# Kernel optimization log

Hardware: AMD Instinct MI355X
Metric: run time of the kernel (lower is better)

## Reference

```python
import jax, jax.numpy as jnp
import numpy as np

TEMPERATURE = 0.5
EPS = 1e-8  # matches torch CosineSimilarity eps


def setup_inputs() -> dict:
    key = jax.random.key(0)
    k1, k2 = jax.random.split(key)
    N, D = 4096, 256
    z1 = jax.random.normal(k1, (N, D), dtype=jnp.float32)
    z2 = jax.random.normal(k2, (N, D), dtype=jnp.float32)
    return {"z1": z1, "z2": z2}


def reference(z1, z2):
    N = z1.shape[0]
    z = jnp.concatenate([z1, z2], axis=0)            # [2N, D]
    norm = jnp.linalg.norm(z, axis=-1, keepdims=True)
    zn = z / jnp.maximum(norm, EPS)                  # L2-normalized
    sim = (zn @ zn.T) / TEMPERATURE                  # [2N, 2N] cosine sim / temp
    # mask self-similarity on the diagonal
    diag = jnp.eye(2 * N, dtype=bool)
    sim = jnp.where(diag, -jnp.inf, sim)
    # positive pair labels: row i pairs with i+N (first half) or i-N (second half)
    labels = jnp.concatenate([jnp.arange(N) + N, jnp.arange(N)])
    logp = jax.nn.log_softmax(sim, axis=-1)
    loss = -jnp.mean(logp[jnp.arange(2 * N), labels])
    return loss
```

## Files before the change

### kernel.cpp

```cpp
#include <hip/hip_runtime.h>
#include <hip/hip_bf16.h>


#define NROWS 8192
#define NHALF 4096
#define DDIM  256

typedef __bf16 bf16;
typedef __bf16 bf16x4 __attribute__((ext_vector_type(4)));
typedef __bf16 bf16x8 __attribute__((ext_vector_type(8)));
typedef float  f32x4  __attribute__((ext_vector_type(4)));

__constant__ const float kTwoLog2e = 2.8853900817779268f;
__constant__ const float kLn2      = 0.6931471805599453f;

__device__ __forceinline__ const float* zrow(const float* z1, const float* z2, int r) {
  return (r < NHALF) ? (z1 + (size_t)r * DDIM) : (z2 + (size_t)(r - NHALF) * DDIM);
}

__global__ void k_normalize(const float* __restrict__ z1, const float* __restrict__ z2,
                            bf16* __restrict__ zn, float* __restrict__ invn,
                            float* __restrict__ rowsum) {
  const int wave = threadIdx.x >> 6, lane = threadIdx.x & 63;
  const int row = blockIdx.x * 4 + wave;
  const float* src = zrow(z1, z2, row);
  f32x4 v = *(const f32x4*)(src + lane * 4);
  float ss = v.x * v.x + v.y * v.y + v.z * v.z + v.w * v.w;
#pragma unroll
  for (int off = 1; off < 64; off <<= 1) ss += __shfl_xor(ss, off);
  const float inv = 1.0f / fmaxf(sqrtf(ss), 1e-8f);
  bf16x4 o;
  o.x = (bf16)(v.x * inv); o.y = (bf16)(v.y * inv);
  o.z = (bf16)(v.z * inv); o.w = (bf16)(v.w * inv);
  *(bf16x4*)(zn + (size_t)row * DDIM + lane * 4) = o;
  if (lane == 0) { invn[row] = inv; rowsum[row] = 0.0f; }
}

#define BMG 256
#define BNG 32
#define CSPLIT 16

typedef const __attribute__((address_space(1))) unsigned int* as1_u32p;
typedef __attribute__((address_space(3))) unsigned int* as3_u32p;

__device__ __forceinline__ void load_lds16(const void* g, void* l) {
  __builtin_amdgcn_global_load_lds((as1_u32p)g, (as3_u32p)l, 16, 0, 0);
}

__global__ __launch_bounds__(256, 2) void k_gram(const bf16* __restrict__ zn,
                                                 float* __restrict__ rowsum) {
  __shared__ __align__(16) unsigned char ldsb[2][BNG * 512];
  const int tid  = threadIdx.x;
  const int wave = tid >> 6, lane = tid & 63;
  const int quad = lane >> 4, l15 = lane & 15;
  const int rowblk = blockIdx.x >> 4, csplit = blockIdx.x & 15;
  const int c0 = csplit * (NROWS / CSPLIT);
  const int iters = (NROWS / CSPLIT) / BNG;

  {
    const unsigned char* src0 = (const unsigned char*)(zn + (size_t)c0 * DDIM);
#pragma unroll
    for (int j = 0; j < 4; ++j) {
      const int p = (wave * 4 + j) * 64 + lane;
      const int r = p >> 5;
      const int q = (p & 31) ^ (r & 7);
      load_lds16(src0 + r * 512 + q * 16, &ldsb[0][(wave * 4 + j) * 1024]);
    }
  }

  const int R0 = rowblk * BMG + wave * 64;
  bf16x8 a[4][8];
#pragma unroll
  for (int s = 0; s < 4; ++s) {
    const bf16x8* ap = (const bf16x8*)(zn + (size_t)(R0 + s * 16 + l15) * DDIM);
#pragma unroll
    for (int kk = 0; kk < 8; ++kk) a[s][kk] = ap[kk * 4 + quad];
  }

  float sum[4][4];
#pragma unroll
  for (int s = 0; s < 4; ++s)
#pragma unroll
    for (int r = 0; r < 4; ++r) sum[s][r] = 0.0f;

  const f32x4 zero4 = {0.f, 0.f, 0.f, 0.f};

  for (int it = 0; it < iters; ++it) {
    __syncthreads();
    const unsigned char* bp = ldsb[it & 1];

    if (it + 1 < iters) {
      const unsigned char* srcn =
          (const unsigned char*)(zn + (size_t)(c0 + (it + 1) * BNG) * DDIM);
#pragma unroll
      for (int j = 0; j < 4; ++j) {
        const int p = (wave * 4 + j) * 64 + lane;
        const int r = p >> 5;
        const int q = (p & 31) ^ (r & 7);
        load_lds16(srcn + r * 512 + q * 16, &ldsb[(it + 1) & 1][(wave * 4 + j) * 1024]);
      }
    }

    f32x4 acc[4][2];
#pragma unroll
    for (int s = 0; s < 4; ++s) { acc[s][0] = zero4; acc[s][1] = zero4; }

#pragma unroll
    for (int kk = 0; kk < 8; ++kk) {
      bf16x8 b[2];
#pragma unroll
      for (int cs = 0; cs < 2; ++cs) {
        const int rb = cs * 16 + l15;
        const int q  = (kk * 4 + quad) ^ (rb & 7);
        b[cs] = *(const bf16x8*)(bp + rb * 512 + q * 16);
      }
#pragma unroll
      for (int s = 0; s < 4; ++s)
#pragma unroll
        for (int cs = 0; cs < 2; ++cs)
          acc[s][cs] =
              __builtin_amdgcn_mfma_f32_16x16x32_bf16(a[s][kk], b[cs], acc[s][cs], 0, 0, 0);
    }

#pragma unroll
    for (int s = 0; s < 4; ++s)
#pragma unroll
      for (int r = 0; r < 4; ++r)
        sum[s][r] += __builtin_amdgcn_exp2f(acc[s][0][r] * kTwoLog2e) +
                     __builtin_amdgcn_exp2f(acc[s][1][r] * kTwoLog2e);
  }

#pragma unroll
  for (int s = 0; s < 4; ++s)
#pragma unroll
    for (int r = 0; r < 4; ++r) {
      float v = sum[s][r];
      v += __shfl_xor(v, 1); v += __shfl_xor(v, 2);
      v += __shfl_xor(v, 4); v += __shfl_xor(v, 8);
      if (l15 == 0)
        atomicAdd(&rowsum[R0 + s * 16 + quad * 4 + r], v);
    }
}

__global__ void k_finalize(const float* __restrict__ z1, const float* __restrict__ z2,
                           const bf16* __restrict__ zn, const float* __restrict__ invn,
                           const float* __restrict__ rowsum, float* __restrict__ contrib) {
  const int wave = threadIdx.x >> 6, lane = threadIdx.x & 63;
  const int row = blockIdx.x * 4 + wave;
  const int pr = (row < NHALF) ? row + NHALF : row - NHALF;

  f32x4 a4 = *(const f32x4*)(zrow(z1, z2, row) + lane * 4);
  f32x4 b4 = *(const f32x4*)(zrow(z1, z2, pr) + lane * 4);
  bf16x4 nb = *(const bf16x4*)(zn + (size_t)row * DDIM + lane * 4);

  float pd = a4.x * b4.x + a4.y * b4.y + a4.z * b4.z + a4.w * b4.w;
  float f0 = (float)nb.x, f1 = (float)nb.y, f2 = (float)nb.z, f3 = (float)nb.w;
  float nd = f0 * f0 + f1 * f1 + f2 * f2 + f3 * f3;
#pragma unroll
  for (int off = 1; off < 64; off <<= 1) {
    pd += __shfl_xor(pd, off);
    nd += __shfl_xor(nd, off);
  }
  if (lane == 0) {
    const float p = 2.0f * pd * invn[row] * invn[pr];
    const float dexp = __builtin_amdgcn_exp2f(kTwoLog2e * nd);
    const float lse = __builtin_amdgcn_logf(rowsum[row] - dexp) * kLn2;
    contrib[row] = lse - p;
  }
}

__global__ void k_reduce(const float* __restrict__ contrib, float* __restrict__ out) {
  const int wave = threadIdx.x >> 6, lane = threadIdx.x & 63;
  float acc = 0.0f;
  for (int i = threadIdx.x; i < NROWS; i += 256) acc += contrib[i];
#pragma unroll
  for (int off = 1; off < 64; off <<= 1) acc += __shfl_xor(acc, off);
  __shared__ float wsum[4];
  if (lane == 0) wsum[wave] = acc;
  __syncthreads();
  if (threadIdx.x == 0)
    out[0] = (wsum[0] + wsum[1] + wsum[2] + wsum[3]) * (1.0f / (float)NROWS);
}

extern "C" void kernel_launch(void* const* d_in, const int* in_sizes, int n_in,
                              void* d_out, int out_size, void* d_ws, size_t ws_size,
                              hipStream_t stream) {
  const float* z1 = (const float*)d_in[0];
  const float* z2 = (const float*)d_in[1];
  unsigned char* ws = (unsigned char*)d_ws;

  bf16* zn = (bf16*)ws;
  float* invn = (float*)(ws + (size_t)NROWS * DDIM * sizeof(bf16));
  float* rowsum = invn + NROWS;
  float* contrib = rowsum + NROWS;

  hipLaunchKernelGGL(k_normalize, dim3(NROWS / 4), dim3(256), 0, stream, z1, z2, zn, invn, rowsum);
  hipLaunchKernelGGL(k_gram, dim3((NROWS / BMG) * CSPLIT), dim3(256), 0, stream, zn, rowsum);
  hipLaunchKernelGGL(k_finalize, dim3(NROWS / 4), dim3(256), 0, stream, z1, z2, zn, invn, rowsum,
                     contrib);
  hipLaunchKernelGGL(k_reduce, dim3(1), dim3(256), 0, stream, contrib, (float*)d_out);
}
```

Baseline: 110.0 us.

## Exploit Gram matrix symmetry with upper-triangular tiles and column-sum atomics

The similarity matrix is symmetric, so the gram kernel now covers only the upper triangle of 128x128 tiles, decoding the tile index with a triangular-number formula. Each off-diagonal tile adds its exponentials both to its row sums and, via transposed column partial sums, to the mirrored rows. This roughly halves the MFMA and exp work. In exchange, blocks are much shorter (four iterations each), the per-block A-fragment load is amortised over less work, and there are more atomic adds to rowsum.

```diff
diff --git a/kernel.cpp b/kernel.cpp
--- a/kernel.cpp
+++ b/kernel.cpp
@@ -36,9 +36,10 @@
   if (lane == 0) { invn[row] = inv; rowsum[row] = 0.0f; }
 }
 
-#define BMG 256
+#define BMG 128
 #define BNG 32
-#define CSPLIT 16
+#define TITERS 4
+#define NTILES 2080
 
 typedef const __attribute__((address_space(1))) unsigned int* as1_u32p;
 typedef __attribute__((address_space(3))) unsigned int* as3_u32p;
@@ -53,12 +54,18 @@
   const int tid  = threadIdx.x;
   const int wave = tid >> 6, lane = tid & 63;
   const int quad = lane >> 4, l15 = lane & 15;
-  const int rowblk = blockIdx.x >> 4, csplit = blockIdx.x & 15;
-  const int c0 = csplit * (NROWS / CSPLIT);
-  const int iters = (NROWS / CSPLIT) / BNG;
+
+  const int kb = blockIdx.x;
+  int I = (int)((129.0f - sqrtf((float)(16641 - 8 * kb))) * 0.5f);
+  while ((I + 1) * (129 - (I + 1)) / 2 <= kb) ++I;
+  while (I * (129 - I) / 2 > kb) --I;
+  const int J = I + (kb - I * (129 - I) / 2);
+  const bool diag = (I == J);
+  const int R0 = I * BMG + wave * 32;
+  const int C0 = J * BMG;
 
   {
-    const unsigned char* src0 = (const unsigned char*)(zn + (size_t)c0 * DDIM);
+    const unsigned char* src0 = (const unsigned char*)(zn + (size_t)C0 * DDIM);
 #pragma unroll
     for (int j = 0; j < 4; ++j) {
       const int p = (wave * 4 + j) * 64 + lane;
@@ -68,30 +75,26 @@
     }
   }
 
-  const int R0 = rowblk * BMG + wave * 64;
-  bf16x8 a[4][8];
-#pragma unroll
-  for (int s = 0; s < 4; ++s) {
+  bf16x8 a[2][8];
+#pragma unroll
+  for (int s = 0; s < 2; ++s) {
     const bf16x8* ap = (const bf16x8*)(zn + (size_t)(R0 + s * 16 + l15) * DDIM);
 #pragma unroll
     for (int kk = 0; kk < 8; ++kk) a[s][kk] = ap[kk * 4 + quad];
   }
 
-  float sum[4][4];
-#pragma unroll
-  for (int s = 0; s < 4; ++s)
-#pragma unroll
-    for (int r = 0; r < 4; ++r) sum[s][r] = 0.0f;
-
+  float sum[2][4] = {{0.f, 0.f, 0.f, 0.f}, {0.f, 0.f, 0.f, 0.f}};
+  float csum[TITERS][2];
   const f32x4 zero4 = {0.f, 0.f, 0.f, 0.f};
 
-  for (int it = 0; it < iters; ++it) {
+#pragma unroll
+  for (int it = 0; it < TITERS; ++it) {
     __syncthreads();
     const unsigned char* bp = ldsb[it & 1];
 
-    if (it + 1 < iters) {
+    if (it + 1 < TITERS) {
       const unsigned char* srcn =
-          (const unsigned char*)(zn + (size_t)(c0 + (it + 1) * BNG) * DDIM);
+          (const unsigned char*)(zn + (size_t)(C0 + (it + 1) * BNG) * DDIM);
 #pragma unroll
       for (int j = 0; j < 4; ++j) {
         const int p = (wave * 4 + j) * 64 + lane;
@@ -101,9 +104,9 @@
       }
     }
 
-    f32x4 acc[4][2];
-#pragma unroll
-    for (int s = 0; s < 4; ++s) { acc[s][0] = zero4; acc[s][1] = zero4; }
+    f32x4 acc[2][2];
+#pragma unroll
+    for (int s = 0; s < 2; ++s) { acc[s][0] = zero4; acc[s][1] = zero4; }
 
 #pragma unroll
     for (int kk = 0; kk < 8; ++kk) {
@@ -115,31 +118,46 @@
         b[cs] = *(const bf16x8*)(bp + rb * 512 + q * 16);
       }
 #pragma unroll
-      for (int s = 0; s < 4; ++s)
+      for (int s = 0; s < 2; ++s)
 #pragma unroll
         for (int cs = 0; cs < 2; ++cs)
           acc[s][cs] =
               __builtin_amdgcn_mfma_f32_16x16x32_bf16(a[s][kk], b[cs], acc[s][cs], 0, 0, 0);
     }
 
-#pragma unroll
-    for (int s = 0; s < 4; ++s)
-#pragma unroll
-      for (int r = 0; r < 4; ++r)
-        sum[s][r] += __builtin_amdgcn_exp2f(acc[s][0][r] * kTwoLog2e) +
-                     __builtin_amdgcn_exp2f(acc[s][1][r] * kTwoLog2e);
-  }
-
-#pragma unroll
-  for (int s = 0; s < 4; ++s)
+    float c0 = 0.f, c1 = 0.f;
+#pragma unroll
+    for (int s = 0; s < 2; ++s)
+#pragma unroll
+      for (int r = 0; r < 4; ++r) {
+        const float e0 = __builtin_amdgcn_exp2f(acc[s][0][r] * kTwoLog2e);
+        const float e1 = __builtin_amdgcn_exp2f(acc[s][1][r] * kTwoLog2e);
+        sum[s][r] += e0 + e1;
+        c0 += e0; c1 += e1;
+      }
+    csum[it][0] = c0; csum[it][1] = c1;
+  }
+
+#pragma unroll
+  for (int s = 0; s < 2; ++s)
 #pragma unroll
     for (int r = 0; r < 4; ++r) {
       float v = sum[s][r];
       v += __shfl_xor(v, 1); v += __shfl_xor(v, 2);
       v += __shfl_xor(v, 4); v += __shfl_xor(v, 8);
-      if (l15 == 0)
-        atomicAdd(&rowsum[R0 + s * 16 + quad * 4 + r], v);
-    }
+      if (l15 == 0) atomicAdd(&rowsum[R0 + s * 16 + quad * 4 + r], v);
+    }
+
+  if (!diag) {
+#pragma unroll
+    for (int it = 0; it < TITERS; ++it)
+#pragma unroll
+      for (int cs = 0; cs < 2; ++cs) {
+        float v = csum[it][cs];
+        v += __shfl_xor(v, 16); v += __shfl_xor(v, 32);
+        if (quad == 0) atomicAdd(&rowsum[C0 + it * BNG + cs * 16 + l15], v);
+      }
+  }
 }
 
 __global__ void k_finalize(const float* __restrict__ z1, const float* __restrict__ z2,
@@ -195,7 +213,7 @@
   float* contrib = rowsum + NROWS;
 
   hipLaunchKernelGGL(k_normalize, dim3(NROWS / 4), dim3(256), 0, stream, z1, z2, zn, invn, rowsum);
-  hipLaunchKernelGGL(k_gram, dim3((NROWS / BMG) * CSPLIT), dim3(256), 0, stream, zn, rowsum);
+  hipLaunchKernelGGL(k_gram, dim3(NTILES), dim3(256), 0, stream, zn, rowsum);
   hipLaunchKernelGGL(k_finalize, dim3(NROWS / 4), dim3(256), 0, stream, z1, z2, zn, invn, rowsum,
                      contrib);
   hipLaunchKernelGGL(k_reduce, dim3(1), dim3(256), 0, stream, contrib, (float*)d_out);
```

Result: slower. 112.4 us (+2.2%).
